# Optimization experiments

Hardware: AMD Instinct MI355X
Metric: run time of the kernel (lower is better)

The kernel has to match this reference:

```python
import jax, jax.numpy as jnp
import numpy as np

NUM_HEAD = 8
HIDDEN = 1024


def setup_inputs() -> dict:
    key = jax.random.key(0)
    ks = jax.random.split(key, 7)
    B, Q, K = 2, 256, 256
    return {
        "query": jax.random.normal(ks[0], (B, Q, HIDDEN), jnp.float32),
        "keys": jax.random.normal(ks[1], (B, K, HIDDEN), jnp.float32),
        "values": jax.random.normal(ks[2], (B, K, HIDDEN), jnp.float32),
        "mask": jax.random.randint(ks[3], (B, K), 0, 2, jnp.int32),
        "W_q": jax.random.normal(ks[4], (HIDDEN, HIDDEN), jnp.float32),
        "W_k": jax.random.normal(ks[5], (HIDDEN, HIDDEN), jnp.float32),
        "V_a": jax.random.normal(ks[6], (HIDDEN,), jnp.float32),
    }


def reference(query, keys, values, mask, W_q, W_k, V_a):
    B, Q, H = query.shape
    K = keys.shape[1]
    h_q = query @ W_q                                   # [B,Q,H]
    h_k = keys @ W_k                                    # [B,K,H]
    # additive (Bahdanau) scores, split hidden into heads and sum per head
    h = jnp.tanh(h_q[:, :, None, :] + h_k[:, None, :, :]) * V_a   # [B,Q,K,H]
    logits = h.reshape(B, Q, K, NUM_HEAD, H // NUM_HEAD).sum(-1)  # [B,Q,K,h]
    logits = jnp.transpose(logits, (0, 3, 1, 2))        # [B,h,Q,K]
    penalty = (1.0 - mask.astype(jnp.float32)) * 99.0   # [B,K]
    logits = logits - penalty[:, None, None, :]
    weights = jax.nn.softmax(logits, axis=-1)           # [B,h,Q,K]
    v = values.reshape(B, K, NUM_HEAD, H // NUM_HEAD)   # [B,K,h,d]
    ctx = jnp.einsum('bhqk,bkhd->bqhd', weights, v).reshape(B, Q, H)
    return ctx, weights
```

## Files before the change

kernel.cpp:

```cpp
#include <hip/hip_runtime.h>
#include <hip/hip_bf16.h>


#define TANH_SCALE 2.88539008177792681472f
#define LOG2E      1.44269504088896340736f

typedef __attribute__((ext_vector_type(8))) short bf16x8_t;
typedef __attribute__((ext_vector_type(4))) float f32x4_t;

__device__ inline ushort bf16_rne(float f) {
  unsigned u = __float_as_uint(f);
  u += 0x7FFFu + ((u >> 16) & 1u);
  return (ushort)(u >> 16);
}
__device__ inline float bf16_to_f(ushort h) { return __uint_as_float((unsigned)h << 16); }
__device__ inline void split1(float v, ushort& hi, ushort& lo) {
  hi = bf16_rne(v);
  lo = bf16_rne(v - bf16_to_f(hi));
}

__global__ __launch_bounds__(256) void split_A(
    const float* __restrict__ query, const float* __restrict__ keys,
    ushort* __restrict__ qhi, ushort* __restrict__ qlo,
    ushort* __restrict__ khi, ushort* __restrict__ klo)
{
  const int z = blockIdx.y;
  const float* in = z ? keys : query;
  ushort* hi = z ? khi : qhi;
  ushort* lo = z ? klo : qlo;
  const size_t i = ((size_t)blockIdx.x * 256 + threadIdx.x) * 4;
  float4 v = *(const float4*)(in + i);
  ushort h0, h1, h2, h3, l0, l1, l2, l3;
  split1(v.x, h0, l0); split1(v.y, h1, l1);
  split1(v.z, h2, l2); split1(v.w, h3, l3);
  *(ushort4*)(hi + i) = make_ushort4(h0, h1, h2, h3);
  *(ushort4*)(lo + i) = make_ushort4(l0, l1, l2, l3);
}

__global__ __launch_bounds__(256) void split_WT(
    const float* __restrict__ Wq, const float* __restrict__ Wk,
    ushort* __restrict__ wqthi, ushort* __restrict__ wqtlo,
    ushort* __restrict__ wkthi, ushort* __restrict__ wktlo)
{
  const int z = blockIdx.z;
  const float* W = z ? Wk : Wq;
  ushort* thi = z ? wkthi : wqthi;
  ushort* tlo = z ? wktlo : wqtlo;
  __shared__ float t[64][65];
  const int tid = threadIdx.x;
  const int n0 = blockIdx.x * 64, h0 = blockIdx.y * 64;
  const int r = tid >> 4, c = (tid & 15) * 4;
#pragma unroll
  for (int i = 0; i < 4; ++i) {
    const int rr = r + i * 16;
    float4 wv = *(const float4*)(W + (size_t)(h0 + rr) * 1024 + n0 + c);
    t[rr][c + 0] = wv.x; t[rr][c + 1] = wv.y;
    t[rr][c + 2] = wv.z; t[rr][c + 3] = wv.w;
  }
  __syncthreads();
#pragma unroll
  for (int i = 0; i < 4; ++i) {
    const int rr = r + i * 16;
    ushort h0v, h1v, h2v, h3v, l0v, l1v, l2v, l3v;
    split1(t[c + 0][rr] * TANH_SCALE, h0v, l0v);
    split1(t[c + 1][rr] * TANH_SCALE, h1v, l1v);
    split1(t[c + 2][rr] * TANH_SCALE, h2v, l2v);
    split1(t[c + 3][rr] * TANH_SCALE, h3v, l3v);
    *(ushort4*)(thi + (size_t)(n0 + rr) * 1024 + h0 + c) = make_ushort4(h0v, h1v, h2v, h3v);
    *(ushort4*)(tlo + (size_t)(n0 + rr) * 1024 + h0 + c) = make_ushort4(l0v, l1v, l2v, l3v);
  }
}

__global__ __launch_bounds__(256) void gemm_mfma(
    const ushort* __restrict__ qhi, const ushort* __restrict__ qlo,
    const ushort* __restrict__ khi, const ushort* __restrict__ klo,
    const ushort* __restrict__ wqthi, const ushort* __restrict__ wqtlo,
    const ushort* __restrict__ wkthi, const ushort* __restrict__ wktlo,
    float* __restrict__ hq_f, float* __restrict__ hkT)
{
  const int z = blockIdx.y;
  const int bid = blockIdx.x;
  int m0, n0, ldc;
  const ushort *Ah_g, *Al_g, *Bh_g, *Bl_g;
  float* C;
  if (z == 0) {
    m0 = (bid >> 4) * 64; n0 = (bid & 15) * 64; ldc = 1024;
    Ah_g = qhi; Al_g = qlo; Bh_g = wqthi; Bl_g = wqtlo; C = hq_f;
  } else {
    m0 = (bid >> 3) * 64; n0 = (bid & 7) * 64; ldc = 512;
    Ah_g = wkthi; Al_g = wktlo; Bh_g = khi; Bl_g = klo; C = hkT;
  }

  __shared__ __align__(16) ushort Ah[64 * 40];
  __shared__ __align__(16) ushort Al[64 * 40];
  __shared__ __align__(16) ushort Bh[64 * 40];
  __shared__ __align__(16) ushort Bl[64 * 40];

  const int tid = threadIdx.x;
  const int srow = tid >> 2, skc = (tid & 3) * 8;
  const size_t gA = (size_t)(m0 + srow) * 1024 + skc;
  const size_t gB = (size_t)(n0 + srow) * 1024 + skc;
  const int soff = srow * 40 + skc;

  uint4 rah = *(const uint4*)(Ah_g + gA);
  uint4 ral = *(const uint4*)(Al_g + gA);
  uint4 rbh = *(const uint4*)(Bh_g + gB);
  uint4 rbl = *(const uint4*)(Bl_g + gB);

  const int w = __builtin_amdgcn_readfirstlane(tid >> 6);
  const int lane = tid & 63;
  const int wm = (w >> 1) * 32, wn = (w & 1) * 32;
  const int fr = lane & 15, kg = lane >> 4;
  const int aoff = (wm + fr) * 40 + kg * 8;
  const int boff = (wn + fr) * 40 + kg * 8;

  f32x4_t acc[2][2] = {};

  for (int kk = 0; kk < 1024; kk += 32) {
    __syncthreads();
    *(uint4*)(Ah + soff) = rah;
    *(uint4*)(Al + soff) = ral;
    *(uint4*)(Bh + soff) = rbh;
    *(uint4*)(Bl + soff) = rbl;
    __syncthreads();

    if (kk + 32 < 1024) {
      rah = *(const uint4*)(Ah_g + gA + kk + 32);
      ral = *(const uint4*)(Al_g + gA + kk + 32);
      rbh = *(const uint4*)(Bh_g + gB + kk + 32);
      rbl = *(const uint4*)(Bl_g + gB + kk + 32);
    }

    bf16x8_t ah0 = *(const bf16x8_t*)(Ah + aoff);
    bf16x8_t ah1 = *(const bf16x8_t*)(Ah + aoff + 16 * 40);
    bf16x8_t al0 = *(const bf16x8_t*)(Al + aoff);
    bf16x8_t al1 = *(const bf16x8_t*)(Al + aoff + 16 * 40);
    bf16x8_t bh0 = *(const bf16x8_t*)(Bh + boff);
    bf16x8_t bh1 = *(const bf16x8_t*)(Bh + boff + 16 * 40);
    bf16x8_t bl0 = *(const bf16x8_t*)(Bl + boff);
    bf16x8_t bl1 = *(const bf16x8_t*)(Bl + boff + 16 * 40);

    acc[0][0] = __builtin_amdgcn_mfma_f32_16x16x32_bf16(ah0, bh0, acc[0][0], 0, 0, 0);
    acc[0][1] = __builtin_amdgcn_mfma_f32_16x16x32_bf16(ah0, bh1, acc[0][1], 0, 0, 0);
    acc[1][0] = __builtin_amdgcn_mfma_f32_16x16x32_bf16(ah1, bh0, acc[1][0], 0, 0, 0);
    acc[1][1] = __builtin_amdgcn_mfma_f32_16x16x32_bf16(ah1, bh1, acc[1][1], 0, 0, 0);
    acc[0][0] = __builtin_amdgcn_mfma_f32_16x16x32_bf16(ah0, bl0, acc[0][0], 0, 0, 0);
    acc[0][1] = __builtin_amdgcn_mfma_f32_16x16x32_bf16(ah0, bl1, acc[0][1], 0, 0, 0);
    acc[1][0] = __builtin_amdgcn_mfma_f32_16x16x32_bf16(ah1, bl0, acc[1][0], 0, 0, 0);
    acc[1][1] = __builtin_amdgcn_mfma_f32_16x16x32_bf16(ah1, bl1, acc[1][1], 0, 0, 0);
    acc[0][0] = __builtin_amdgcn_mfma_f32_16x16x32_bf16(al0, bh0, acc[0][0], 0, 0, 0);
    acc[0][1] = __builtin_amdgcn_mfma_f32_16x16x32_bf16(al0, bh1, acc[0][1], 0, 0, 0);
    acc[1][0] = __builtin_amdgcn_mfma_f32_16x16x32_bf16(al1, bh0, acc[1][0], 0, 0, 0);
    acc[1][1] = __builtin_amdgcn_mfma_f32_16x16x32_bf16(al1, bh1, acc[1][1], 0, 0, 0);
  }

#pragma unroll
  for (int fm = 0; fm < 2; ++fm)
#pragma unroll
    for (int fn = 0; fn < 2; ++fn) {
      const int col = n0 + wn + fn * 16 + fr;
#pragma unroll
      for (int j = 0; j < 4; ++j) {
        const int row = m0 + wm + fm * 16 + kg * 4 + j;
        C[(size_t)row * ldc + col] = acc[fm][fn][j];
      }
    }
}

#define COMP(vk, hq0v, hq1v, vad)                                     \
  {                                                                   \
    float e0 = __builtin_amdgcn_exp2f(hq0v + vk.x);                   \
    float e1 = __builtin_amdgcn_exp2f(hq0v + vk.y);                   \
    float e2 = __builtin_amdgcn_exp2f(hq0v + vk.z);                   \
    float e3 = __builtin_amdgcn_exp2f(hq0v + vk.w);                   \
    acc00 += vad * __builtin_amdgcn_rcpf(e0 + 1.0f);                  \
    acc01 += vad * __builtin_amdgcn_rcpf(e1 + 1.0f);                  \
    acc02 += vad * __builtin_amdgcn_rcpf(e2 + 1.0f);                  \
    acc03 += vad * __builtin_amdgcn_rcpf(e3 + 1.0f);                  \
    float f0 = __builtin_amdgcn_exp2f(hq1v + vk.x);                   \
    float f1 = __builtin_amdgcn_exp2f(hq1v + vk.y);                   \
    float f2 = __builtin_amdgcn_exp2f(hq1v + vk.z);                   \
    float f3 = __builtin_amdgcn_exp2f(hq1v + vk.w);                   \
    acc10 += vad * __builtin_amdgcn_rcpf(f0 + 1.0f);                  \
    acc11 += vad * __builtin_amdgcn_rcpf(f1 + 1.0f);                  \
    acc12 += vad * __builtin_amdgcn_rcpf(f2 + 1.0f);                  \
    acc13 += vad * __builtin_amdgcn_rcpf(f3 + 1.0f);                  \
  }

__global__ __launch_bounds__(256) void logits_v3(
    const float* __restrict__ hq_f, const float* __restrict__ hkT,
    const float* __restrict__ Va, const int* __restrict__ mask,
    float* __restrict__ logits)
{
  const int tid = threadIdx.x;
  const int lane = tid & 63;
  const int w = __builtin_amdgcn_readfirstlane(tid >> 6);
  const int bid = blockIdx.x;
  const int hb = bid >> 5;
  const int b = hb & 1, h = hb >> 1;
  const int qb = (bid & 31) * 4 + w;
  const int q0 = qb * 2;

  int4 mk = *(const int4*)(mask + b * 256 + 4 * lane);
  const float pen0 = 99.0f * (1.0f - (float)mk.x);
  const float pen1 = 99.0f * (1.0f - (float)mk.y);
  const float pen2 = 99.0f * (1.0f - (float)mk.z);
  const float pen3 = 99.0f * (1.0f - (float)mk.w);

  float ssum = Va[h * 128 + lane] + Va[h * 128 + 64 + lane];
#pragma unroll
  for (int off = 32; off; off >>= 1) ssum += __shfl_xor(ssum, off, 64);

  const float* hkbase = hkT + (size_t)(h * 128) * 512 + b * 256 + 4 * lane;
  const float* hqr0 = hq_f + (size_t)(b * 256 + q0) * 1024 + h * 128;
  const float* hqr1 = hqr0 + 1024;
  const float* vap = Va + h * 128;

  float acc00 = 0.f, acc01 = 0.f, acc02 = 0.f, acc03 = 0.f;
  float acc10 = 0.f, acc11 = 0.f, acc12 = 0.f, acc13 = 0.f;

  float4 vk0 = *(const float4*)(hkbase + 0 * 512);
  float4 vk1 = *(const float4*)(hkbase + 1 * 512);
  float4 vk2 = *(const float4*)(hkbase + 2 * 512);
  float4 vk3 = *(const float4*)(hkbase + 3 * 512);
  float4 hqA = *(const float4*)(hqr0);
  float4 hqB = *(const float4*)(hqr1);
  float4 va4 = *(const float4*)(vap);

  for (int g = 0; g < 32; ++g) {
    float4 nvk0, nvk1, nvk2, nvk3, nhqA, nhqB, nva4;
    if (g < 31) {
      const float* hb2 = hkbase + (size_t)(4 * g + 4) * 512;
      nvk0 = *(const float4*)(hb2 + 0 * 512);
      nvk1 = *(const float4*)(hb2 + 1 * 512);
      nvk2 = *(const float4*)(hb2 + 2 * 512);
      nvk3 = *(const float4*)(hb2 + 3 * 512);
      nhqA = *(const float4*)(hqr0 + 4 * g + 4);
      nhqB = *(const float4*)(hqr1 + 4 * g + 4);
      nva4 = *(const float4*)(vap + 4 * g + 4);
    }
    COMP(vk0, hqA.x, hqB.x, va4.x);
    COMP(vk1, hqA.y, hqB.y, va4.y);
    COMP(vk2, hqA.z, hqB.z, va4.z);
    COMP(vk3, hqA.w, hqB.w, va4.w);
    if (g < 31) {
      vk0 = nvk0; vk1 = nvk1; vk2 = nvk2; vk3 = nvk3;
      hqA = nhqA; hqB = nhqB; va4 = nva4;
    }
  }

  float* lp = logits + ((size_t)((b * 8 + h) * 256) + q0) * 256 + 4 * lane;
  float4 o0, o1;
  o0.x = ssum - 2.0f * acc00 - pen0;
  o0.y = ssum - 2.0f * acc01 - pen1;
  o0.z = ssum - 2.0f * acc02 - pen2;
  o0.w = ssum - 2.0f * acc03 - pen3;
  o1.x = ssum - 2.0f * acc10 - pen0;
  o1.y = ssum - 2.0f * acc11 - pen1;
  o1.z = ssum - 2.0f * acc12 - pen2;
  o1.w = ssum - 2.0f * acc13 - pen3;
  *(float4*)(lp) = o0;
  *(float4*)(lp + 256) = o1;
}

__global__ __launch_bounds__(256) void softmax_pv(
    const float* __restrict__ values,
    float* __restrict__ weights,
    float* __restrict__ ctx)
{
  __shared__ __align__(16) float w_lds[8 * 256];
  const int tid = threadIdx.x;
  const int b = blockIdx.z, h = blockIdx.y, q0 = blockIdx.x * 8;
  const int wave = tid >> 6, lane = tid & 63;

#pragma unroll
  for (int r = 0; r < 2; ++r) {
    const int row = wave * 2 + r;
    float* lp = &weights[((size_t)(b * 8 + h) * 256 + q0 + row) * 256];
    float4 L = *(const float4*)&lp[lane * 4];
    float m = fmaxf(fmaxf(L.x, L.y), fmaxf(L.z, L.w));
#pragma unroll
    for (int off = 32; off; off >>= 1) m = fmaxf(m, __shfl_xor(m, off, 64));
    float4 P;
    P.x = __builtin_amdgcn_exp2f((L.x - m) * LOG2E);
    P.y = __builtin_amdgcn_exp2f((L.y - m) * LOG2E);
    P.z = __builtin_amdgcn_exp2f((L.z - m) * LOG2E);
    P.w = __builtin_amdgcn_exp2f((L.w - m) * LOG2E);
    float s = (P.x + P.y) + (P.z + P.w);
#pragma unroll
    for (int off = 32; off; off >>= 1) s += __shfl_xor(s, off, 64);
    float inv = 1.0f / s;
    P.x *= inv; P.y *= inv; P.z *= inv; P.w *= inv;
    *(float4*)&w_lds[row * 256 + lane * 4] = P;
    *(float4*)&lp[lane * 4] = P;
  }
  __syncthreads();

  const int q = tid >> 5, dq = tid & 31;
  const float* vb = values + (size_t)(b * 256) * 1024 + h * 128 + dq * 4;
  const float* wrow = w_lds + q * 256;
  float4 accE = make_float4(0, 0, 0, 0), accO = make_float4(0, 0, 0, 0);
#pragma unroll 4
  for (int k = 0; k < 256; k += 2) {
    float4 v0 = *(const float4*)&vb[k * 1024];
    float4 v1 = *(const float4*)&vb[(k + 1) * 1024];
    float w0 = wrow[k], w1 = wrow[k + 1];
    accE.x += w0 * v0.x; accE.y += w0 * v0.y; accE.z += w0 * v0.z; accE.w += w0 * v0.w;
    accO.x += w1 * v1.x; accO.y += w1 * v1.y; accO.z += w1 * v1.z; accO.w += w1 * v1.w;
  }
  float4 o;
  o.x = accE.x + accO.x; o.y = accE.y + accO.y; o.z = accE.z + accO.z; o.w = accE.w + accO.w;
  *(float4*)&ctx[(size_t)(b * 256 + q0 + q) * 1024 + h * 128 + dq * 4] = o;
}

extern "C" void kernel_launch(void* const* d_in, const int* in_sizes, int n_in,
                              void* d_out, int out_size, void* d_ws, size_t ws_size,
                              hipStream_t stream) {
  const float* query  = (const float*)d_in[0];
  const float* keys   = (const float*)d_in[1];
  const float* values = (const float*)d_in[2];
  const int*   mask   = (const int*)d_in[3];
  const float* Wq     = (const float*)d_in[4];
  const float* Wk     = (const float*)d_in[5];
  const float* Va     = (const float*)d_in[6];

  float* ctx     = (float*)d_out;
  float* weights = ctx + 524288;

  ushort* qhi   = (ushort*)d_ws;
  ushort* qlo   = qhi + 524288;
  ushort* khi   = qlo + 524288;
  ushort* klo   = khi + 524288;
  ushort* wqthi = klo + 524288;
  ushort* wqtlo = wqthi + 1048576;
  ushort* wkthi = wqtlo + 1048576;
  ushort* wktlo = wkthi + 1048576;
  float*  hq_f  = (float*)(wktlo + 1048576);
  float*  hkT   = hq_f + 524288;

  split_A <<<dim3(512, 2), 256, 0, stream>>>(query, keys, qhi, qlo, khi, klo);
  split_WT<<<dim3(16, 16, 2), 256, 0, stream>>>(Wq, Wk, wqthi, wqtlo, wkthi, wktlo);
  gemm_mfma<<<dim3(128, 2), 256, 0, stream>>>(qhi, qlo, khi, klo,
                                              wqthi, wqtlo, wkthi, wktlo, hq_f, hkT);
  logits_v3<<<dim3(512), 256, 0, stream>>>(hq_f, hkT, Va, mask, weights);
  softmax_pv<<<dim3(32, 8, 2), 256, 0, stream>>>(values, weights, ctx);
}
```

Measured before the change: 77.56 us.

## Fuse split kernels into one prep launch and fuse logits with softmax-PV

Merges the two input-splitting kernels into a single launch with a block-index branch. It also fuses the logits kernel with softmax and the P·V product, so each block computes logits for 8 query rows, does the softmax in registers, stages the weights in LDS and then computes the context. This drops two kernel launches and the round-trip of the logits through global memory. The trade-off is a longer fused kernel that carries extra LDS and register pressure.

```diff
diff --git a/kernel.cpp b/kernel.cpp
--- a/kernel.cpp
+++ b/kernel.cpp
@@ -19,55 +19,55 @@
   lo = bf16_rne(v - bf16_to_f(hi));
 }
 
-__global__ __launch_bounds__(256) void split_A(
+__global__ __launch_bounds__(256) void prep(
     const float* __restrict__ query, const float* __restrict__ keys,
+    const float* __restrict__ Wq, const float* __restrict__ Wk,
     ushort* __restrict__ qhi, ushort* __restrict__ qlo,
-    ushort* __restrict__ khi, ushort* __restrict__ klo)
-{
-  const int z = blockIdx.y;
-  const float* in = z ? keys : query;
-  ushort* hi = z ? khi : qhi;
-  ushort* lo = z ? klo : qlo;
-  const size_t i = ((size_t)blockIdx.x * 256 + threadIdx.x) * 4;
-  float4 v = *(const float4*)(in + i);
-  ushort h0, h1, h2, h3, l0, l1, l2, l3;
-  split1(v.x, h0, l0); split1(v.y, h1, l1);
-  split1(v.z, h2, l2); split1(v.w, h3, l3);
-  *(ushort4*)(hi + i) = make_ushort4(h0, h1, h2, h3);
-  *(ushort4*)(lo + i) = make_ushort4(l0, l1, l2, l3);
-}
-
-__global__ __launch_bounds__(256) void split_WT(
-    const float* __restrict__ Wq, const float* __restrict__ Wk,
+    ushort* __restrict__ khi, ushort* __restrict__ klo,
     ushort* __restrict__ wqthi, ushort* __restrict__ wqtlo,
     ushort* __restrict__ wkthi, ushort* __restrict__ wktlo)
 {
-  const int z = blockIdx.z;
-  const float* W = z ? Wk : Wq;
-  ushort* thi = z ? wkthi : wqthi;
-  ushort* tlo = z ? wktlo : wqtlo;
   __shared__ float t[64][65];
-  const int tid = threadIdx.x;
-  const int n0 = blockIdx.x * 64, h0 = blockIdx.y * 64;
-  const int r = tid >> 4, c = (tid & 15) * 4;
-#pragma unroll
-  for (int i = 0; i < 4; ++i) {
-    const int rr = r + i * 16;
-    float4 wv = *(const float4*)(W + (size_t)(h0 + rr) * 1024 + n0 + c);
-    t[rr][c + 0] = wv.x; t[rr][c + 1] = wv.y;
-    t[rr][c + 2] = wv.z; t[rr][c + 3] = wv.w;
-  }
-  __syncthreads();
-#pragma unroll
-  for (int i = 0; i < 4; ++i) {
-    const int rr = r + i * 16;
-    ushort h0v, h1v, h2v, h3v, l0v, l1v, l2v, l3v;
-    split1(t[c + 0][rr] * TANH_SCALE, h0v, l0v);
-    split1(t[c + 1][rr] * TANH_SCALE, h1v, l1v);
-    split1(t[c + 2][rr] * TANH_SCALE, h2v, l2v);
-    split1(t[c + 3][rr] * TANH_SCALE, h3v, l3v);
-    *(ushort4*)(thi + (size_t)(n0 + rr) * 1024 + h0 + c) = make_ushort4(h0v, h1v, h2v, h3v);
-    *(ushort4*)(tlo + (size_t)(n0 + rr) * 1024 + h0 + c) = make_ushort4(l0v, l1v, l2v, l3v);
+  const int bid = blockIdx.x, tid = threadIdx.x;
+  if (bid < 1024) {
+    const int z = bid >> 9;
+    const float* in = z ? keys : query;
+    ushort* hi = z ? khi : qhi;
+    ushort* lo = z ? klo : qlo;
+    const size_t i = ((size_t)(bid & 511) * 256 + tid) * 4;
+    float4 v = *(const float4*)(in + i);
+    ushort h0, h1, h2, h3, l0, l1, l2, l3;
+    split1(v.x, h0, l0); split1(v.y, h1, l1);
+    split1(v.z, h2, l2); split1(v.w, h3, l3);
+    *(ushort4*)(hi + i) = make_ushort4(h0, h1, h2, h3);
+    *(ushort4*)(lo + i) = make_ushort4(l0, l1, l2, l3);
+  } else {
+    const int idx = bid - 1024;
+    const int z = idx >> 8;
+    const float* W = z ? Wk : Wq;
+    ushort* thi = z ? wkthi : wqthi;
+    ushort* tlo = z ? wktlo : wqtlo;
+    const int n0 = (idx & 15) * 64, h0 = ((idx >> 4) & 15) * 64;
+    const int r = tid >> 4, c = (tid & 15) * 4;
+#pragma unroll
+    for (int i = 0; i < 4; ++i) {
+      const int rr = r + i * 16;
+      float4 wv = *(const float4*)(W + (size_t)(h0 + rr) * 1024 + n0 + c);
+      t[rr][c + 0] = wv.x; t[rr][c + 1] = wv.y;
+      t[rr][c + 2] = wv.z; t[rr][c + 3] = wv.w;
+    }
+    __syncthreads();
+#pragma unroll
+    for (int i = 0; i < 4; ++i) {
+      const int rr = r + i * 16;
+      ushort h0v, h1v, h2v, h3v, l0v, l1v, l2v, l3v;
+      split1(t[c + 0][rr] * TANH_SCALE, h0v, l0v);
+      split1(t[c + 1][rr] * TANH_SCALE, h1v, l1v);
+      split1(t[c + 2][rr] * TANH_SCALE, h2v, l2v);
+      split1(t[c + 3][rr] * TANH_SCALE, h3v, l3v);
+      *(ushort4*)(thi + (size_t)(n0 + rr) * 1024 + h0 + c) = make_ushort4(h0v, h1v, h2v, h3v);
+      *(ushort4*)(tlo + (size_t)(n0 + rr) * 1024 + h0 + c) = make_ushort4(l0v, l1v, l2v, l3v);
+    }
   }
 }
 
@@ -187,19 +187,21 @@
     acc13 += vad * __builtin_amdgcn_rcpf(f3 + 1.0f);                  \
   }
 
-__global__ __launch_bounds__(256) void logits_v3(
+__global__ __launch_bounds__(256) void attn_fused(
     const float* __restrict__ hq_f, const float* __restrict__ hkT,
     const float* __restrict__ Va, const int* __restrict__ mask,
-    float* __restrict__ logits)
+    const float* __restrict__ values,
+    float* __restrict__ weights, float* __restrict__ ctx)
 {
+  __shared__ __align__(16) float w_lds[8 * 256];
   const int tid = threadIdx.x;
   const int lane = tid & 63;
   const int w = __builtin_amdgcn_readfirstlane(tid >> 6);
   const int bid = blockIdx.x;
   const int hb = bid >> 5;
   const int b = hb & 1, h = hb >> 1;
-  const int qb = (bid & 31) * 4 + w;
-  const int q0 = qb * 2;
+  const int qt = (bid & 31) * 8;
+  const int q0 = qt + w * 2;
 
   int4 mk = *(const int4*)(mask + b * 256 + 4 * lane);
   const float pen0 = 99.0f * (1.0f - (float)mk.x);
@@ -249,51 +251,48 @@
     }
   }
 
-  float* lp = logits + ((size_t)((b * 8 + h) * 256) + q0) * 256 + 4 * lane;
-  float4 o0, o1;
-  o0.x = ssum - 2.0f * acc00 - pen0;
-  o0.y = ssum - 2.0f * acc01 - pen1;
-  o0.z = ssum - 2.0f * acc02 - pen2;
-  o0.w = ssum - 2.0f * acc03 - pen3;
-  o1.x = ssum - 2.0f * acc10 - pen0;
-  o1.y = ssum - 2.0f * acc11 - pen1;
-  o1.z = ssum - 2.0f * acc12 - pen2;
-  o1.w = ssum - 2.0f * acc13 - pen3;
-  *(float4*)(lp) = o0;
-  *(float4*)(lp + 256) = o1;
-}
-
-__global__ __launch_bounds__(256) void softmax_pv(
-    const float* __restrict__ values,
-    float* __restrict__ weights,
-    float* __restrict__ ctx)
-{
-  __shared__ __align__(16) float w_lds[8 * 256];
-  const int tid = threadIdx.x;
-  const int b = blockIdx.z, h = blockIdx.y, q0 = blockIdx.x * 8;
-  const int wave = tid >> 6, lane = tid & 63;
-
-#pragma unroll
-  for (int r = 0; r < 2; ++r) {
-    const int row = wave * 2 + r;
-    float* lp = &weights[((size_t)(b * 8 + h) * 256 + q0 + row) * 256];
-    float4 L = *(const float4*)&lp[lane * 4];
-    float m = fmaxf(fmaxf(L.x, L.y), fmaxf(L.z, L.w));
-#pragma unroll
-    for (int off = 32; off; off >>= 1) m = fmaxf(m, __shfl_xor(m, off, 64));
-    float4 P;
-    P.x = __builtin_amdgcn_exp2f((L.x - m) * LOG2E);
-    P.y = __builtin_amdgcn_exp2f((L.y - m) * LOG2E);
-    P.z = __builtin_amdgcn_exp2f((L.z - m) * LOG2E);
-    P.w = __builtin_amdgcn_exp2f((L.w - m) * LOG2E);
-    float s = (P.x + P.y) + (P.z + P.w);
-#pragma unroll
-    for (int off = 32; off; off >>= 1) s += __shfl_xor(s, off, 64);
-    float inv = 1.0f / s;
-    P.x *= inv; P.y *= inv; P.z *= inv; P.w *= inv;
-    *(float4*)&w_lds[row * 256 + lane * 4] = P;
-    *(float4*)&lp[lane * 4] = P;
-  }
+  float4 L0, L1;
+  L0.x = ssum - 2.0f * acc00 - pen0;
+  L0.y = ssum - 2.0f * acc01 - pen1;
+  L0.z = ssum - 2.0f * acc02 - pen2;
+  L0.w = ssum - 2.0f * acc03 - pen3;
+  L1.x = ssum - 2.0f * acc10 - pen0;
+  L1.y = ssum - 2.0f * acc11 - pen1;
+  L1.z = ssum - 2.0f * acc12 - pen2;
+  L1.w = ssum - 2.0f * acc13 - pen3;
+
+  float m0 = fmaxf(fmaxf(L0.x, L0.y), fmaxf(L0.z, L0.w));
+  float m1 = fmaxf(fmaxf(L1.x, L1.y), fmaxf(L1.z, L1.w));
+#pragma unroll
+  for (int off = 32; off; off >>= 1) {
+    m0 = fmaxf(m0, __shfl_xor(m0, off, 64));
+    m1 = fmaxf(m1, __shfl_xor(m1, off, 64));
+  }
+  float4 P0, P1;
+  P0.x = __builtin_amdgcn_exp2f((L0.x - m0) * LOG2E);
+  P0.y = __builtin_amdgcn_exp2f((L0.y - m0) * LOG2E);
+  P0.z = __builtin_amdgcn_exp2f((L0.z - m0) * LOG2E);
+  P0.w = __builtin_amdgcn_exp2f((L0.w - m0) * LOG2E);
+  P1.x = __builtin_amdgcn_exp2f((L1.x - m1) * LOG2E);
+  P1.y = __builtin_amdgcn_exp2f((L1.y - m1) * LOG2E);
+  P1.z = __builtin_amdgcn_exp2f((L1.z - m1) * LOG2E);
+  P1.w = __builtin_amdgcn_exp2f((L1.w - m1) * LOG2E);
+  float s0 = (P0.x + P0.y) + (P0.z + P0.w);
+  float s1 = (P1.x + P1.y) + (P1.z + P1.w);
+#pragma unroll
+  for (int off = 32; off; off >>= 1) {
+    s0 += __shfl_xor(s0, off, 64);
+    s1 += __shfl_xor(s1, off, 64);
+  }
+  float inv0 = 1.0f / s0, inv1 = 1.0f / s1;
+  P0.x *= inv0; P0.y *= inv0; P0.z *= inv0; P0.w *= inv0;
+  P1.x *= inv1; P1.y *= inv1; P1.z *= inv1; P1.w *= inv1;
+
+  float* wp = weights + ((size_t)((b * 8 + h) * 256) + q0) * 256 + 4 * lane;
+  *(float4*)(wp) = P0;
+  *(float4*)(wp + 256) = P1;
+  *(float4*)&w_lds[(w * 2 + 0) * 256 + 4 * lane] = P0;
+  *(float4*)&w_lds[(w * 2 + 1) * 256 + 4 * lane] = P1;
   __syncthreads();
 
   const int q = tid >> 5, dq = tid & 31;
@@ -310,7 +309,7 @@
   }
   float4 o;
   o.x = accE.x + accO.x; o.y = accE.y + accO.y; o.z = accE.z + accO.z; o.w = accE.w + accO.w;
-  *(float4*)&ctx[(size_t)(b * 256 + q0 + q) * 1024 + h * 128 + dq * 4] = o;
+  *(float4*)&ctx[(size_t)(b * 256 + qt + q) * 1024 + h * 128 + dq * 4] = o;
 }
 
 extern "C" void kernel_launch(void* const* d_in, const int* in_sizes, int n_in,
@@ -338,10 +337,10 @@
   float*  hq_f  = (float*)(wktlo + 1048576);
   float*  hkT   = hq_f + 524288;
 
-  split_A <<<dim3(512, 2), 256, 0, stream>>>(query, keys, qhi, qlo, khi, klo);
-  split_WT<<<dim3(16, 16, 2), 256, 0, stream>>>(Wq, Wk, wqthi, wqtlo, wkthi, wktlo);
+  prep<<<dim3(1536), 256, 0, stream>>>(query, keys, Wq, Wk,
+                                       qhi, qlo, khi, klo,
+                                       wqthi, wqtlo, wkthi, wktlo);
   gemm_mfma<<<dim3(128, 2), 256, 0, stream>>>(qhi, qlo, khi, klo,
                                               wqthi, wqtlo, wkthi, wktlo, hq_f, hkT);
-  logits_v3<<<dim3(512), 256, 0, stream>>>(hq_f, hkT, Va, mask, weights);
-  softmax_pv<<<dim3(32, 8, 2), 256, 0, stream>>>(values, weights, ctx);
-}
+  attn_fused<<<dim3(512), 256, 0, stream>>>(hq_f, hkT, Va, mask, values, weights, ctx);
+}
```

After: 73.10 us. -5.7%, faster.
